# Kernel optimization log

Measured on AMD Instinct MI355X. Metric: run time of the kernel, lower is better.

Reference implementation:

```python
import jax, jax.numpy as jnp
import numpy as np

OUT_FEATURES = 4096
IN_FEATURES = 4096
GROUP_SIZE = 128
NUM_GROUPS = IN_FEATURES // GROUP_SIZE  # 32
PACKED_SIZE = OUT_FEATURES * IN_FEATURES // 8  # 2097152


def setup_inputs() -> dict:
    key = jax.random.key(0)
    k1, k2, k3, k4 = jax.random.split(key, 4)
    x = jax.random.normal(k1, (2, 512, IN_FEATURES), dtype=jnp.float32)
    # random packed 4-bit weights (8 nibbles per int32)
    w_packed = jax.random.randint(k2, (PACKED_SIZE,), jnp.iinfo(jnp.int32).min,
                                  jnp.iinfo(jnp.int32).max, dtype=jnp.int32)
    w_scale = jax.random.uniform(k3, (OUT_FEATURES, NUM_GROUPS), dtype=jnp.float32) * 0.05
    w_zero = jax.random.randint(k4, (OUT_FEATURES, NUM_GROUPS), 0, 8, dtype=jnp.int32)
    return {"x": x, "w_packed": w_packed, "w_scale": w_scale, "w_zero": w_zero}


def _unpack_dequant(w_packed, w_scale, w_zero):
    # Extract 8 nibbles per int32: (v >> (i*4)) & 0xF, i = 0..7
    shifts = jnp.arange(8, dtype=jnp.int32) * 4
    nibbles = (w_packed[:, None] >> shifts[None, :]) & 15  # [packed, 8]
    w4 = nibbles.reshape(-1)  # [out*in], values 0..15
    w4 = jnp.where(w4 >= 8, w4 - 16, w4)  # signed 4-bit -> [-8, 7]
    w_int = w4.reshape(OUT_FEATURES, NUM_GROUPS, GROUP_SIZE).astype(jnp.float32)
    # per-(row, group) dequant: (q - zero) * scale
    w = (w_int - w_zero[:, :, None].astype(jnp.float32)) * w_scale[:, :, None]
    return w.reshape(OUT_FEATURES, IN_FEATURES)


def reference(x, w_packed, w_scale, w_zero):
    weight = _unpack_dequant(w_packed, w_scale, w_zero).astype(x.dtype)
    # F.linear: y = x @ W^T
    return jnp.einsum('bsi,oi->bso', x, weight)
```

## Files before the change

kernel.cpp:

```cpp
#include <hip/hip_runtime.h>
#include <stdint.h>

#define IN_F 4096
#define OUT_F 4096
#define NG 32

typedef __attribute__((ext_vector_type(8))) _Float16 half8;
typedef __attribute__((ext_vector_type(2))) _Float16 half2t;
typedef __attribute__((ext_vector_type(4))) float floatx4;

__global__ __launch_bounds__(256) void prep_kernel(
    const float* __restrict__ x, _Float16* __restrict__ Xh,
    const float* __restrict__ wscale, const int* __restrict__ wzero,
    uint2* __restrict__ SZ, int nxb) {
  int b = blockIdx.x;
  if (b < nxb) {
    int i = b * 256 + threadIdx.x;
    const float4* x4 = (const float4*)x;
    float4 a = x4[2 * i];
    float4 c = x4[2 * i + 1];
    uint4 o;
    o.x = __builtin_bit_cast(unsigned, __builtin_amdgcn_cvt_pkrtz(a.x, c.x));
    o.y = __builtin_bit_cast(unsigned, __builtin_amdgcn_cvt_pkrtz(a.y, c.y));
    o.z = __builtin_bit_cast(unsigned, __builtin_amdgcn_cvt_pkrtz(a.z, c.z));
    o.w = __builtin_bit_cast(unsigned, __builtin_amdgcn_cvt_pkrtz(a.w, c.w));
    ((uint4*)Xh)[i] = o;
  } else {
    int i = (b - nxb) * 256 + threadIdx.x;
    float s = wscale[i];
    int zp = wzero[i];
    _Float16 sh = (_Float16)s;
    _Float16 ch = (_Float16)(float)(1032 + zp);
    unsigned s2 = (unsigned)__builtin_bit_cast(unsigned short, sh) * 0x10001u;
    unsigned c2 = (unsigned)__builtin_bit_cast(unsigned short, ch) * 0x10001u;
    SZ[i] = make_uint2(s2, c2);
  }
}

#define NSTEP 32

__device__ __forceinline__ uint4 dequant8(unsigned v, uint2 szv) {
  unsigned tx = v ^ 0x88888888u;
  half2t s2 = __builtin_bit_cast(half2t, szv.x);
  half2t c2 = __builtin_bit_cast(half2t, szv.y);
  unsigned p0 = (tx & 0x000F000Fu) | 0x64006400u;
  unsigned p1 = ((tx >> 4) & 0x000F000Fu) | 0x64006400u;
  unsigned p2 = ((tx >> 8) & 0x000F000Fu) | 0x64006400u;
  unsigned p3 = ((tx >> 12) & 0x000F000Fu) | 0x64006400u;
  half2t w0 = (__builtin_bit_cast(half2t, p0) - c2) * s2;
  half2t w1 = (__builtin_bit_cast(half2t, p1) - c2) * s2;
  half2t w2 = (__builtin_bit_cast(half2t, p2) - c2) * s2;
  half2t w3 = (__builtin_bit_cast(half2t, p3) - c2) * s2;
  uint4 o;
  o.x = __builtin_bit_cast(unsigned, w0);
  o.y = __builtin_bit_cast(unsigned, w1);
  o.z = __builtin_bit_cast(unsigned, w2);
  o.w = __builtin_bit_cast(unsigned, w3);
  return o;
}

__global__ __launch_bounds__(512, 2) void gemm_fused(
    const _Float16* __restrict__ A, const int* __restrict__ wp,
    const uint2* __restrict__ SZ, float* __restrict__ out,
    int M, int N, int K) {
  __shared__ __align__(16) _Float16 Alds[4 * 8192];
  __shared__ __align__(16) _Float16 Blds[4 * 8192];

  int t = threadIdx.x;
  int wave = t >> 6, lane = t & 63;
  int h = wave >> 2, w2 = wave & 3;
  int wm = (w2 >> 1) * 64, wn = (w2 & 1) * 64;
  int r = lane & 15, quad = lane >> 4, rb = r & 7;
  int bm = blockIdx.y * 128, bn = blockIdx.x * 128;

  floatx4 acc[4][4] = {};

  int kc = t & 7;
  int row0 = t >> 3;
  int row1 = row0 + 64;
  int gkc = kc ^ (row0 & 7);

  const _Float16* Ag = A + (size_t)bm * K;
  const _Float16* gA[4];
  gA[0] = Ag + (size_t)row0 * K + gkc * 8;
  gA[1] = Ag + (size_t)row1 * K + gkc * 8;
  gA[2] = gA[0] + 2048;
  gA[3] = gA[1] + 2048;

  const int* gB[4];
  const uint2* gS[4];
  gB[0] = wp + (size_t)(bn + row0) * (IN_F / 8) + kc;
  gB[1] = wp + (size_t)(bn + row1) * (IN_F / 8) + kc;
  gB[2] = gB[0] + 256;
  gB[3] = gB[1] + 256;
  gS[0] = SZ + (size_t)(bn + row0) * NG;
  gS[1] = SZ + (size_t)(bn + row1) * NG;
  gS[2] = gS[0] + 16;
  gS[3] = gS[1] + 16;

  int bslot = gkc << 3;
  int bofs0 = row0 * 64 + bslot;
  int bofs1 = row1 * 64 + bslot;

  auto STAGE_A = [&](int i, int buf) {
#pragma unroll
    for (int j = 0; j < 4; ++j) {
      const _Float16* src = gA[j] + i * 64;
      int dst = ((j >> 1) * 2 + buf) * 8192 + (t + 512 * (j & 1)) * 8;
      __builtin_amdgcn_global_load_lds(
          (const __attribute__((address_space(1))) void*)src,
          (__attribute__((address_space(3))) void*)(&Alds[dst]), 16, 0, 0);
    }
  };
  auto STAGE_B = [&](const unsigned* v, const uint2* sz, int buf) {
#pragma unroll
    for (int j = 0; j < 4; ++j) {
      int ofs = ((j >> 1) * 2 + buf) * 8192 + ((j & 1) ? bofs1 : bofs0);
      *(uint4*)&Blds[ofs] = dequant8(v[j], sz[j]);
    }
  };
  auto LOADV = [&](int i, unsigned* v, uint2* sz) {
#pragma unroll
    for (int j = 0; j < 4; ++j) {
      v[j] = (unsigned)gB[j][i * 8];
      sz[j] = gS[j][i >> 1];
    }
  };

  unsigned v[4];
  uint2 sz[4];
  LOADV(0, v, sz);
  STAGE_A(0, 0);
  STAGE_B(v, sz, 0);
  LOADV(1, v, sz);
  __syncthreads();

  int cur = 0;
  for (int i = 0; i < NSTEP; ++i) {
    int nxt = cur ^ 1;
    if (i + 1 < NSTEP) {
      STAGE_A(i + 1, nxt);
      STAGE_B(v, sz, nxt);
      int i2 = (i + 2 < NSTEP) ? (i + 2) : (NSTEP - 1);
      LOADV(i2, v, sz);
    }

    const _Float16* Ab = &Alds[(h * 2 + cur) * 8192];
    const _Float16* Bb = &Blds[(h * 2 + cur) * 8192];
#pragma unroll
    for (int ks = 0; ks < 2; ++ks) {
      half8 af[4], bf[4];
#pragma unroll
      for (int mi = 0; mi < 4; ++mi) {
        int R = wm + mi * 16 + r;
        af[mi] = *(const half8*)&Ab[R * 64 + (((ks * 4 + quad) ^ rb) << 3)];
      }
#pragma unroll
      for (int ni = 0; ni < 4; ++ni) {
        int R = wn + ni * 16 + r;
        bf[ni] = *(const half8*)&Bb[R * 64 + (((ks * 4 + quad) ^ rb) << 3)];
      }
#pragma unroll
      for (int mi = 0; mi < 4; ++mi)
#pragma unroll
        for (int ni = 0; ni < 4; ++ni)
          acc[mi][ni] = __builtin_amdgcn_mfma_f32_16x16x32_f16(
              af[mi], bf[ni], acc[mi][ni], 0, 0, 0);
    }
    __syncthreads();
    cur = nxt;
  }

  floatx4* red = (floatx4*)Alds;
  if (h == 1) {
#pragma unroll
    for (int mi = 0; mi < 4; ++mi)
#pragma unroll
      for (int ni = 0; ni < 4; ++ni)
        red[(mi * 4 + ni) * 256 + w2 * 64 + lane] = acc[mi][ni];
  }
  __syncthreads();
  if (h == 0) {
#pragma unroll
    for (int mi = 0; mi < 4; ++mi) {
#pragma unroll
      for (int ni = 0; ni < 4; ++ni) {
        acc[mi][ni] += red[(mi * 4 + ni) * 256 + w2 * 64 + lane];
#pragma unroll
        for (int i = 0; i < 4; ++i) {
          int grow = bm + wm + mi * 16 + quad * 4 + i;
          int gcol = bn + wn + ni * 16 + r;
          out[(size_t)grow * N + gcol] = acc[mi][ni][i];
        }
      }
    }
  }
}

extern "C" void kernel_launch(void* const* d_in, const int* in_sizes, int n_in,
                              void* d_out, int out_size, void* d_ws, size_t ws_size,
                              hipStream_t stream) {
  const float* x = (const float*)d_in[0];
  const int* wp = (const int*)d_in[1];
  const float* wscale = (const float*)d_in[2];
  const int* wzero = (const int*)d_in[3];
  float* out = (float*)d_out;

  int M = in_sizes[0] / IN_F;

  _Float16* Xh = (_Float16*)d_ws;
  uint2* SZ = (uint2*)((char*)d_ws + (size_t)M * IN_F * 2);

  int nxb = (M * IN_F / 8) / 256;
  int nzb = (OUT_F * NG) / 256;
  prep_kernel<<<nxb + nzb, 256, 0, stream>>>(x, Xh, wscale, wzero, SZ, nxb);

  dim3 grid(OUT_F / 128, M / 128);
  gemm_fused<<<grid, 512, 0, stream>>>(Xh, wp, SZ, out, M, OUT_F, IN_F);
}
```

Before: 122.5 us.

## Replace intra-block K split with grid split-K and atomic accumulation

Drops the 512-thread block that split K across two wave halves and reduced through LDS. It now launches 256-thread blocks over a 3D grid with split-K of 4, and each block atomically adds its partial tile into an output that is memset to zero first. This gives four times as many blocks for better occupancy and CU fill, and the LDS footprint shrinks because double buffering is removed. In exchange it adds a memset, float atomic traffic to the output, and nondeterministic summation order, and it loses the overlap of loads with MFMA that double buffering provided.

```diff
diff --git a/kernel.cpp b/kernel.cpp
--- a/kernel.cpp
+++ b/kernel.cpp
@@ -4,10 +4,16 @@
 #define IN_F 4096
 #define OUT_F 4096
 #define NG 32
+#define SPLITK 4
+#define NSTEP 16
 
 typedef __attribute__((ext_vector_type(8))) _Float16 half8;
 typedef __attribute__((ext_vector_type(2))) _Float16 half2t;
 typedef __attribute__((ext_vector_type(4))) float floatx4;
+
+__device__ __forceinline__ unsigned pkh(float a, float b) {
+  return __builtin_bit_cast(unsigned, __builtin_amdgcn_cvt_pkrtz(a, b));
+}
 
 __global__ __launch_bounds__(256) void prep_kernel(
     const float* __restrict__ x, _Float16* __restrict__ Xh,
@@ -20,10 +26,10 @@
     float4 a = x4[2 * i];
     float4 c = x4[2 * i + 1];
     uint4 o;
-    o.x = __builtin_bit_cast(unsigned, __builtin_amdgcn_cvt_pkrtz(a.x, c.x));
-    o.y = __builtin_bit_cast(unsigned, __builtin_amdgcn_cvt_pkrtz(a.y, c.y));
-    o.z = __builtin_bit_cast(unsigned, __builtin_amdgcn_cvt_pkrtz(a.z, c.z));
-    o.w = __builtin_bit_cast(unsigned, __builtin_amdgcn_cvt_pkrtz(a.w, c.w));
+    o.x = pkh(a.x, c.x);
+    o.y = pkh(a.y, c.y);
+    o.z = pkh(a.z, c.z);
+    o.w = pkh(a.w, c.w);
     ((uint4*)Xh)[i] = o;
   } else {
     int i = (b - nxb) * 256 + threadIdx.x;
@@ -36,8 +42,6 @@
     SZ[i] = make_uint2(s2, c2);
   }
 }
-
-#define NSTEP 32
 
 __device__ __forceinline__ uint4 dequant8(unsigned v, uint2 szv) {
   unsigned tx = v ^ 0x88888888u;
@@ -59,106 +63,79 @@
   return o;
 }
 
-__global__ __launch_bounds__(512, 2) void gemm_fused(
+__global__ __launch_bounds__(256, 4) void gemm_fused(
     const _Float16* __restrict__ A, const int* __restrict__ wp,
     const uint2* __restrict__ SZ, float* __restrict__ out,
     int M, int N, int K) {
-  __shared__ __align__(16) _Float16 Alds[4 * 8192];
-  __shared__ __align__(16) _Float16 Blds[4 * 8192];
+  __shared__ __align__(16) _Float16 Alds[128 * 64];
+  __shared__ __align__(16) _Float16 Blds[128 * 64];
 
-  int t = threadIdx.x;
-  int wave = t >> 6, lane = t & 63;
-  int h = wave >> 2, w2 = wave & 3;
-  int wm = (w2 >> 1) * 64, wn = (w2 & 1) * 64;
-  int r = lane & 15, quad = lane >> 4, rb = r & 7;
-  int bm = blockIdx.y * 128, bn = blockIdx.x * 128;
+  const int t = threadIdx.x;
+  const int wave = t >> 6, lane = t & 63;
+  const int wm = (wave >> 1) * 64, wn = (wave & 1) * 64;
+  const int r = lane & 15, quad = lane >> 4, rb = r & 7;
+  const int bm = blockIdx.y * 128, bn = blockIdx.x * 128;
+  const int kz = blockIdx.z * (K / SPLITK);
 
   floatx4 acc[4][4] = {};
 
-  int kc = t & 7;
-  int row0 = t >> 3;
-  int row1 = row0 + 64;
-  int gkc = kc ^ (row0 & 7);
+  const int row = t >> 3, kc = t & 7;
+  const int gkc = kc ^ (row & 7);
 
-  const _Float16* Ag = A + (size_t)bm * K;
   const _Float16* gA[4];
-  gA[0] = Ag + (size_t)row0 * K + gkc * 8;
-  gA[1] = Ag + (size_t)row1 * K + gkc * 8;
-  gA[2] = gA[0] + 2048;
-  gA[3] = gA[1] + 2048;
-
   const int* gB[4];
   const uint2* gS[4];
-  gB[0] = wp + (size_t)(bn + row0) * (IN_F / 8) + kc;
-  gB[1] = wp + (size_t)(bn + row1) * (IN_F / 8) + kc;
-  gB[2] = gB[0] + 256;
-  gB[3] = gB[1] + 256;
-  gS[0] = SZ + (size_t)(bn + row0) * NG;
-  gS[1] = SZ + (size_t)(bn + row1) * NG;
-  gS[2] = gS[0] + 16;
-  gS[3] = gS[1] + 16;
+  int bofs[4];
+#pragma unroll
+  for (int j = 0; j < 4; ++j) {
+    int rj = row + 32 * j;
+    gA[j] = A + (size_t)(bm + rj) * K + kz + gkc * 8;
+    gB[j] = wp + (size_t)(bn + rj) * (IN_F / 8) + (kz >> 3) + kc;
+    gS[j] = SZ + (size_t)(bn + rj) * NG + (kz >> 7);
+    bofs[j] = rj * 64 + ((kc ^ (row & 7)) << 3);
+  }
 
-  int bslot = gkc << 3;
-  int bofs0 = row0 * 64 + bslot;
-  int bofs1 = row1 * 64 + bslot;
+  unsigned v[4];
+  uint2 sv[4];
+#define LOADV(i)                                                              \
+  {                                                                           \
+    _Pragma("unroll") for (int j = 0; j < 4; ++j) {                           \
+      v[j] = (unsigned)gB[j][(i) * 8];                                        \
+      sv[j] = gS[j][(i) >> 1];                                                \
+    }                                                                         \
+  }
 
-  auto STAGE_A = [&](int i, int buf) {
+  LOADV(0);
+  for (int i = 0; i < NSTEP; ++i) {
+    __syncthreads();
+
 #pragma unroll
     for (int j = 0; j < 4; ++j) {
       const _Float16* src = gA[j] + i * 64;
-      int dst = ((j >> 1) * 2 + buf) * 8192 + (t + 512 * (j & 1)) * 8;
       __builtin_amdgcn_global_load_lds(
           (const __attribute__((address_space(1))) void*)src,
-          (__attribute__((address_space(3))) void*)(&Alds[dst]), 16, 0, 0);
+          (__attribute__((address_space(3))) void*)(&Alds[(t + 256 * j) * 8]),
+          16, 0, 0);
     }
-  };
-  auto STAGE_B = [&](const unsigned* v, const uint2* sz, int buf) {
 #pragma unroll
-    for (int j = 0; j < 4; ++j) {
-      int ofs = ((j >> 1) * 2 + buf) * 8192 + ((j & 1) ? bofs1 : bofs0);
-      *(uint4*)&Blds[ofs] = dequant8(v[j], sz[j]);
-    }
-  };
-  auto LOADV = [&](int i, unsigned* v, uint2* sz) {
-#pragma unroll
-    for (int j = 0; j < 4; ++j) {
-      v[j] = (unsigned)gB[j][i * 8];
-      sz[j] = gS[j][i >> 1];
-    }
-  };
+    for (int j = 0; j < 4; ++j)
+      *(uint4*)&Blds[bofs[j]] = dequant8(v[j], sv[j]);
+    if (i + 1 < NSTEP) LOADV(i + 1);
 
-  unsigned v[4];
-  uint2 sz[4];
-  LOADV(0, v, sz);
-  STAGE_A(0, 0);
-  STAGE_B(v, sz, 0);
-  LOADV(1, v, sz);
-  __syncthreads();
+    __syncthreads();
 
-  int cur = 0;
-  for (int i = 0; i < NSTEP; ++i) {
-    int nxt = cur ^ 1;
-    if (i + 1 < NSTEP) {
-      STAGE_A(i + 1, nxt);
-      STAGE_B(v, sz, nxt);
-      int i2 = (i + 2 < NSTEP) ? (i + 2) : (NSTEP - 1);
-      LOADV(i2, v, sz);
-    }
-
-    const _Float16* Ab = &Alds[(h * 2 + cur) * 8192];
-    const _Float16* Bb = &Blds[(h * 2 + cur) * 8192];
 #pragma unroll
     for (int ks = 0; ks < 2; ++ks) {
       half8 af[4], bf[4];
 #pragma unroll
       for (int mi = 0; mi < 4; ++mi) {
         int R = wm + mi * 16 + r;
-        af[mi] = *(const half8*)&Ab[R * 64 + (((ks * 4 + quad) ^ rb) << 3)];
+        af[mi] = *(const half8*)&Alds[R * 64 + (((ks * 4 + quad) ^ rb) << 3)];
       }
 #pragma unroll
       for (int ni = 0; ni < 4; ++ni) {
         int R = wn + ni * 16 + r;
-        bf[ni] = *(const half8*)&Bb[R * 64 + (((ks * 4 + quad) ^ rb) << 3)];
+        bf[ni] = *(const half8*)&Blds[R * 64 + (((ks * 4 + quad) ^ rb) << 3)];
       }
 #pragma unroll
       for (int mi = 0; mi < 4; ++mi)
@@ -167,31 +144,17 @@
           acc[mi][ni] = __builtin_amdgcn_mfma_f32_16x16x32_f16(
               af[mi], bf[ni], acc[mi][ni], 0, 0, 0);
     }
-    __syncthreads();
-    cur = nxt;
   }
 
-  floatx4* red = (floatx4*)Alds;
-  if (h == 1) {
 #pragma unroll
-    for (int mi = 0; mi < 4; ++mi)
+  for (int mi = 0; mi < 4; ++mi) {
 #pragma unroll
-      for (int ni = 0; ni < 4; ++ni)
-        red[(mi * 4 + ni) * 256 + w2 * 64 + lane] = acc[mi][ni];
-  }
-  __syncthreads();
-  if (h == 0) {
+    for (int ni = 0; ni < 4; ++ni) {
 #pragma unroll
-    for (int mi = 0; mi < 4; ++mi) {
-#pragma unroll
-      for (int ni = 0; ni < 4; ++ni) {
-        acc[mi][ni] += red[(mi * 4 + ni) * 256 + w2 * 64 + lane];
-#pragma unroll
-        for (int i = 0; i < 4; ++i) {
-          int grow = bm + wm + mi * 16 + quad * 4 + i;
-          int gcol = bn + wn + ni * 16 + r;
-          out[(size_t)grow * N + gcol] = acc[mi][ni][i];
-        }
+      for (int i2 = 0; i2 < 4; ++i2) {
+        int grow = bm + wm + mi * 16 + quad * 4 + i2;
+        int gcol = bn + wn + ni * 16 + r;
+        unsafeAtomicAdd(&out[(size_t)grow * N + gcol], acc[mi][ni][i2]);
       }
     }
   }
@@ -211,10 +174,12 @@
   _Float16* Xh = (_Float16*)d_ws;
   uint2* SZ = (uint2*)((char*)d_ws + (size_t)M * IN_F * 2);
 
+  hipMemsetAsync(out, 0, (size_t)M * OUT_F * sizeof(float), stream);
+
   int nxb = (M * IN_F / 8) / 256;
   int nzb = (OUT_F * NG) / 256;
   prep_kernel<<<nxb + nzb, 256, 0, stream>>>(x, Xh, wscale, wzero, SZ, nxb);
 
-  dim3 grid(OUT_F / 128, M / 128);
-  gemm_fused<<<grid, 512, 0, stream>>>(Xh, wp, SZ, out, M, OUT_F, IN_F);
+  dim3 grid(OUT_F / 128, M / 128, SPLITK);
+  gemm_fused<<<grid, 256, 0, stream>>>(Xh, wp, SZ, out, M, OUT_F, IN_F);
 }
```

Result: slower. 165.3 us (+34.9%).
